# Optimization experiments

Hardware: AMD Instinct MI355X
Metric: run time of the kernel (lower is better)

## Reference

```python
import jax, jax.numpy as jnp
import numpy as np

EPS = 1e-12  # torch F.normalize clamp epsilon
NOISE = np.array([1e-05, 2e-05, 3e-05], dtype=np.float32)  # diagonal regularizer


def setup_inputs() -> dict:
    key = jax.random.key(0)
    B, C = 65536, 128
    v_feat = jax.random.normal(key, (B, C, 3), dtype=jnp.float32)
    return {"v_feat": v_feat}


def reference(v_feat):
    # L2 normalize each 3-vector (B, C, 3) along last dim
    norm = jnp.sqrt(jnp.sum(v_feat * v_feat, axis=-1, keepdims=True))
    v = v_feat / jnp.maximum(norm, EPS)

    # Covariance M = v^T v  -> (B, 3, 3), plus tiny diagonal noise for stability
    M = jnp.einsum('bci,bcj->bij', v, v) + jnp.diag(jnp.asarray(NOISE))[None, :, :]

    # Batched symmetric 3x3 eigendecomposition (ascending eigenvalues)
    _, evecs = jnp.linalg.eigh(M)  # evecs: (B, 3, 3), columns are eigenvectors
    v1 = evecs[:, :, 0]  # (B, 3)
    v2 = evecs[:, :, 1]

    # Sign disambiguation: align with the mean direction of the features
    def fix_sign(vec):
        s = jnp.sign(jnp.sum(v * vec[:, None, :], axis=(1, 2)))  # (B,)
        s = jnp.where(s == 0, 1.0, s)
        return vec * s[:, None]

    v1 = fix_sign(v1)
    v2 = fix_sign(v2)
    v3 = jnp.cross(v1, v2)

    # Frame: columns [v1 v2 v3] -> (B, 3, 3)
    return jnp.stack([v1, v2, v3], axis=-1)
```

## Files before the change

### kernel.cpp

```cpp
#include <hip/hip_runtime.h>
#include <math.h>
#include <stdint.h>


#define BLOCK 256
#define BPB   32

template <int CTRL>
__device__ __forceinline__ float ror16_f32(float v) {
    union { float f; int i; } u, r;
    u.f = v;
    r.i = __builtin_amdgcn_mov_dpp(u.i, CTRL, 0xF, 0xF, true);
    return r.f;
}

__device__ __forceinline__ float frsqrt(float x) {
    float r = __builtin_amdgcn_rsqf(x);
    return r * fmaf(-0.5f * x, r * r, 1.5f);
}
__device__ __forceinline__ float frcp(float x) {
    float r = __builtin_amdgcn_rcpf(x);
    return r * fmaf(-x, r, 2.0f);
}

template <int P, int Q, int R>
__device__ __forceinline__ void jrot(float (&A)[3][3], float (&V)[3][3]) {
    float apq = A[P][Q];
    if (fabsf(apq) > 1e-12f) {
        float theta = (A[Q][Q] - A[P][P]) * 0.5f * frcp(apq);
        float q = fmaf(theta, theta, 1.0f);
        float sq = q * frsqrt(q);
        float t = frcp(fabsf(theta) + sq);
        if (theta < 0.0f) t = -t;
        float c = frsqrt(fmaf(t, t, 1.0f));
        float s = t * c;
        float apq_t = t * apq;
        A[P][P] = A[P][P] - apq_t;
        A[Q][Q] = A[Q][Q] + apq_t;
        A[P][Q] = 0.0f;
        A[Q][P] = 0.0f;
        float apr = A[P][R], aqr = A[Q][R];
        A[P][R] = fmaf(c, apr, -s * aqr); A[R][P] = A[P][R];
        A[Q][R] = fmaf(s, apr,  c * aqr); A[R][Q] = A[Q][R];
#pragma unroll
        for (int i = 0; i < 3; ++i) {
            float vip = V[i][P], viq = V[i][Q];
            V[i][P] = fmaf(c, vip, -s * viq);
            V[i][Q] = fmaf(s, vip,  c * viq);
        }
    }
}

__device__ __forceinline__ void accum8(const float4 (&q)[6], float (&m)[8]) {
    float f[24];
#pragma unroll
    for (int i = 0; i < 6; ++i) {
        f[4 * i + 0] = q[i].x; f[4 * i + 1] = q[i].y;
        f[4 * i + 2] = q[i].z; f[4 * i + 3] = q[i].w;
    }
#pragma unroll
    for (int k = 0; k < 8; ++k) {
        float fx = f[3 * k + 0];
        float fy = f[3 * k + 1];
        float fz = f[3 * k + 2];
        float n2 = fmaf(fx, fx, fmaf(fy, fy, fz * fz));
        float inv = __builtin_amdgcn_rsqf(fmaxf(n2, 1e-24f));
        float x = fx * inv;
        float y = fy * inv;
        float z = fz * inv;
        m[0] = fmaf(x, x, m[0]);
        m[1] = fmaf(x, y, m[1]);
        m[2] = fmaf(x, z, m[2]);
        m[3] = fmaf(y, y, m[3]);
        m[4] = fmaf(y, z, m[4]);
        m[5] += x; m[6] += y; m[7] += z;
    }
}

__device__ __forceinline__ void reduce16(float (&m)[8]) {
#pragma unroll
    for (int k = 0; k < 8; ++k) m[k] += ror16_f32<0x121>(m[k]);
#pragma unroll
    for (int k = 0; k < 8; ++k) m[k] += ror16_f32<0x122>(m[k]);
#pragma unroll
    for (int k = 0; k < 8; ++k) m[k] += ror16_f32<0x124>(m[k]);
#pragma unroll
    for (int k = 0; k < 8; ++k) m[k] += ror16_f32<0x128>(m[k]);
}

__global__ __launch_bounds__(BLOCK) void vn_fused(
    const float* __restrict__ vf, float* __restrict__ out, int B) {
    __shared__ __align__(16) float sA[BPB][9];

    const int tid  = threadIdx.x;
    const int wave = tid >> 6;
    const int lane = tid & 63;
    const int g    = lane >> 4;
    const int sub  = lane & 15;

    const int blockBase = blockIdx.x * BPB;
    const int slotA = wave * 8 + g;
    const int slotB = wave * 8 + 4 + g;
    const int bA = blockBase + slotA;
    const int bB = blockBase + slotB;

    float4 qa[6], qb[6];
    if (bA < B) {
        const float4* pa =
            reinterpret_cast<const float4*>(vf + (size_t)bA * 384 + sub * 24);
#pragma unroll
        for (int i = 0; i < 6; ++i) qa[i] = pa[i];
    }
    if (bB < B) {
        const float4* pb =
            reinterpret_cast<const float4*>(vf + (size_t)bB * 384 + sub * 24);
#pragma unroll
        for (int i = 0; i < 6; ++i) qb[i] = pb[i];
    }

    if (bA < B) {
        float m[8];
#pragma unroll
        for (int k = 0; k < 8; ++k) m[k] = 0.0f;
        accum8(qa, m);
        reduce16(m);
        if (sub == 0) {
#pragma unroll
            for (int k = 0; k < 8; ++k) sA[slotA][k] = m[k];
        }
    }
    if (bB < B) {
        float m[8];
#pragma unroll
        for (int k = 0; k < 8; ++k) m[k] = 0.0f;
        accum8(qb, m);
        reduce16(m);
        if (sub == 0) {
#pragma unroll
            for (int k = 0; k < 8; ++k) sA[slotB][k] = m[k];
        }
    }

    __syncthreads();

    if (tid < BPB) {
        const int b = blockBase + tid;
        if (b < B) {
            float m[8];
#pragma unroll
            for (int k = 0; k < 8; ++k) m[k] = sA[tid][k];

            float A[3][3], V[3][3];
            A[0][0] = m[0] + 1e-05f;
            A[0][1] = m[1]; A[1][0] = m[1];
            A[0][2] = m[2]; A[2][0] = m[2];
            A[1][1] = m[3] + 2e-05f;
            A[1][2] = m[4]; A[2][1] = m[4];
            A[2][2] = (128.0f - m[0] - m[3]) + 3e-05f;
#pragma unroll
            for (int i = 0; i < 3; ++i)
#pragma unroll
                for (int j = 0; j < 3; ++j) V[i][j] = (i == j) ? 1.0f : 0.0f;

#pragma unroll
            for (int sweep = 0; sweep < 4; ++sweep) {
                jrot<0, 1, 2>(A, V);
                jrot<0, 2, 1>(A, V);
                jrot<1, 2, 0>(A, V);
            }

            float e0 = A[0][0], e1 = A[1][1], e2 = A[2][2];
            float c0x = V[0][0], c0y = V[1][0], c0z = V[2][0];
            float c1x = V[0][1], c1y = V[1][1], c1z = V[2][1];
            float c2x = V[0][2], c2y = V[1][2], c2z = V[2][2];

#define CSWAP(ea, eb, ax, ay, az, bx, by, bz)                         \
            if (ea > eb) {                                            \
                float t_;                                             \
                t_ = ea; ea = eb; eb = t_;                            \
                t_ = ax; ax = bx; bx = t_;                            \
                t_ = ay; ay = by; by = t_;                            \
                t_ = az; az = bz; bz = t_;                            \
            }
            CSWAP(e0, e1, c0x, c0y, c0z, c1x, c1y, c1z)
            CSWAP(e1, e2, c1x, c1y, c1z, c2x, c2y, c2z)
            CSWAP(e0, e1, c0x, c0y, c0z, c1x, c1y, c1z)
#undef CSWAP

            float s0 = m[5], s1 = m[6], s2 = m[7];
            float d1 = s0 * c0x + s1 * c0y + s2 * c0z;
            float f1 = (d1 < 0.0f) ? -1.0f : 1.0f;
            c0x *= f1; c0y *= f1; c0z *= f1;
            float d2 = s0 * c1x + s1 * c1y + s2 * c1z;
            float f2 = (d2 < 0.0f) ? -1.0f : 1.0f;
            c1x *= f2; c1y *= f2; c1z *= f2;

            float v3x = c0y * c1z - c0z * c1y;
            float v3y = c0z * c1x - c0x * c1z;
            float v3z = c0x * c1y - c0y * c1x;

            sA[tid][0] = c0x; sA[tid][1] = c1x; sA[tid][2] = v3x;
            sA[tid][3] = c0y; sA[tid][4] = c1y; sA[tid][5] = v3y;
            sA[tid][6] = c0z; sA[tid][7] = c1z; sA[tid][8] = v3z;
        }
    }

    __syncthreads();

    if (blockBase + BPB <= B) {
        if (tid < 72) {
            const float4* s4 = reinterpret_cast<const float4*>(&sA[0][0]);
            float4* o4 = reinterpret_cast<float4*>(out + (size_t)blockBase * 9);
            o4[tid] = s4[tid];
        }
    } else if (tid < BPB) {
        const int b = blockBase + tid;
        if (b < B) {
            float* o = out + (size_t)b * 9;
#pragma unroll
            for (int k = 0; k < 9; ++k) o[k] = sA[tid][k];
        }
    }
}

extern "C" void kernel_launch(void* const* d_in, const int* in_sizes, int n_in,
                              void* d_out, int out_size, void* d_ws, size_t ws_size,
                              hipStream_t stream) {
    const float* vf = (const float*)d_in[0];
    float* out = (float*)d_out;
    const int B = in_sizes[0] / 384;
    const int grid = (B + BPB - 1) / BPB;
    vn_fused<<<dim3(grid), dim3(BLOCK), 0, stream>>>(vf, out, B);
}
```

Baseline: 24.88 us.

## Double-buffer feature loads and process 64 batches per block

Each block now covers 64 batch elements instead of 32. Each wave iterates four times, prefetching the next batch element's features into a second register buffer while reducing the current one. This aims to overlap global-memory latency with compute and to amortize the serial per-block eigen-solve and output write. In exchange the grid is half as large, the loads for a wave are serialized across iterations rather than all issued up front, and the eigen stage now runs on a full wave of 64 threads.

```diff
diff --git a/kernel.cpp b/kernel.cpp
--- a/kernel.cpp
+++ b/kernel.cpp
@@ -4,7 +4,8 @@
 
 
 #define BLOCK 256
-#define BPB   32
+#define BPB   64
+#define NIT   4
 
 template <int CTRL>
 __device__ __forceinline__ float ror16_f32(float v) {
@@ -99,45 +100,41 @@
     const int sub  = lane & 15;
 
     const int blockBase = blockIdx.x * BPB;
-    const int slotA = wave * 8 + g;
-    const int slotB = wave * 8 + 4 + g;
-    const int bA = blockBase + slotA;
-    const int bB = blockBase + slotB;
-
-    float4 qa[6], qb[6];
-    if (bA < B) {
-        const float4* pa =
-            reinterpret_cast<const float4*>(vf + (size_t)bA * 384 + sub * 24);
-#pragma unroll
-        for (int i = 0; i < 6; ++i) qa[i] = pa[i];
-    }
-    if (bB < B) {
-        const float4* pb =
-            reinterpret_cast<const float4*>(vf + (size_t)bB * 384 + sub * 24);
-#pragma unroll
-        for (int i = 0; i < 6; ++i) qb[i] = pb[i];
-    }
-
-    if (bA < B) {
-        float m[8];
-#pragma unroll
-        for (int k = 0; k < 8; ++k) m[k] = 0.0f;
-        accum8(qa, m);
-        reduce16(m);
-        if (sub == 0) {
-#pragma unroll
-            for (int k = 0; k < 8; ++k) sA[slotA][k] = m[k];
-        }
-    }
-    if (bB < B) {
-        float m[8];
-#pragma unroll
-        for (int k = 0; k < 8; ++k) m[k] = 0.0f;
-        accum8(qb, m);
-        reduce16(m);
-        if (sub == 0) {
-#pragma unroll
-            for (int k = 0; k < 8; ++k) sA[slotB][k] = m[k];
+    const int slot0 = wave * (4 * NIT) + g;
+
+    auto loadq = [&](int b, float4 (&q)[6]) {
+        const float4* p =
+            reinterpret_cast<const float4*>(vf + (size_t)b * 384 + sub * 24);
+#pragma unroll
+        for (int i = 0; i < 6; ++i) q[i] = p[i];
+    };
+
+    float4 q0[6], q1[6];
+    {
+        const int b0 = blockBase + slot0;
+        if (b0 < B) loadq(b0, q0);
+    }
+
+#pragma unroll
+    for (int it = 0; it < NIT; ++it) {
+        float4 (&qc)[6] = (it & 1) ? q1 : q0;
+        float4 (&qn)[6] = (it & 1) ? q0 : q1;
+        const int slot = slot0 + it * 4;
+        const int b = blockBase + slot;
+        if (it + 1 < NIT) {
+            const int bn = b + 4;
+            if (bn < B) loadq(bn, qn);
+        }
+        if (b < B) {
+            float m[8];
+#pragma unroll
+            for (int k = 0; k < 8; ++k) m[k] = 0.0f;
+            accum8(qc, m);
+            reduce16(m);
+            if (sub == 0) {
+#pragma unroll
+                for (int k = 0; k < 8; ++k) sA[slot][k] = m[k];
+            }
         }
     }
 
@@ -208,7 +205,7 @@
     __syncthreads();
 
     if (blockBase + BPB <= B) {
-        if (tid < 72) {
+        if (tid < (BPB * 9) / 4) {
             const float4* s4 = reinterpret_cast<const float4*>(&sA[0][0]);
             float4* o4 = reinterpret_cast<float4*>(out + (size_t)blockBase * 9);
             o4[tid] = s4[tid];
```

Result: no change. 24.61 us (-1.1%).
